# Performance work log

Hardware: AMD Instinct MI355X
Metric: run time of the kernel (lower is better)

## Reference

```python
import jax, jax.numpy as jnp
import numpy as np

SD, MD, HM, HR, N_STEPS = 64, 64, 128, 128, 10
N_VARS, DEG = 2048, 8


def _build_graph():
    rng = np.random.default_rng(0)
    n = N_VARS
    us = np.repeat(np.arange(n), 4)
    ks = np.tile(np.arange(1, 5), n)
    vs = (us + ks) % n
    factors = np.stack([np.minimum(us, vs), np.maximum(us, vs)], 1)  # [F,2], u<v
    F = factors.shape[0]
    J = np.zeros((n, n), np.float32)
    vals = rng.normal(size=F).astype(np.float32)
    J[factors[:, 0], factors[:, 1]] = vals
    J[factors[:, 1], factors[:, 0]] = vals
    b = rng.normal(size=n).astype(np.float32)
    var_node = factors.reshape(-1)          # variable of each message node
    fac_node = np.repeat(np.arange(F), 2)   # factor of each message node
    M = var_node.shape[0]
    order = np.argsort(var_node, kind='stable').reshape(n, DEG)
    jj = np.broadcast_to(order[:, :, None], (n, DEG, DEG))
    ii = np.broadcast_to(order[:, None, :], (n, DEG, DEG))
    mask = fac_node[jj] != fac_node[ii]     # same variable, different factor
    f2v_row = jj[mask].astype(np.int64)
    f2v_col = ii[mask].astype(np.int64)
    fu = fac_node[f2v_row]; fv = fac_node[f2v_col]
    feat5 = np.stack([b[var_node[f2v_col]],
                      J[factors[fu, 0], factors[fu, 1]], J[factors[fu, 1], factors[fu, 0]],
                      J[factors[fv, 0], factors[fv, 1]], J[factors[fv, 1], factors[fv, 0]]], 1).astype(np.float32)
    v2f_row = np.arange(M, dtype=np.int64)
    v2f_col = v2f_row ^ 1                   # same factor, other variable
    f = fac_node[v2f_row]
    feat4 = np.stack([b[var_node[v2f_row]], b[var_node[v2f_col]],
                      J[factors[f, 0], factors[f, 1]], J[factors[f, 1], factors[f, 0]]], 1).astype(np.float32)
    return f2v_row, f2v_col, feat5, v2f_row, v2f_col, feat4, var_node.astype(np.int64), M


def setup_inputs():
    f2v_row, f2v_col, feat5, v2f_row, v2f_col, feat4, readout_col, M = _build_graph()
    rng = np.random.default_rng(1)
    def lin(o, i):
        return rng.normal(0, 0.1, size=(o, i)).astype(np.float32), np.zeros(o, np.float32)
    def gru_p():
        s = 1.0 / np.sqrt(SD)
        return tuple(rng.uniform(-s, s, sh).astype(np.float32)
                     for sh in ((3 * SD, MD), (3 * SD, SD), (3 * SD,), (3 * SD,)))
    d = {}
    d['attn_W'], d['attn_b'] = lin(1, 2 * SD)
    d['v2f_W1'], d['v2f_b1'] = lin(HM, 2 * SD + 5)
    d['v2f_W2'], d['v2f_b2'] = lin(HM, HM)
    d['v2f_W3'], d['v2f_b3'] = lin(MD, HM)
    d['f2v_W1'], d['f2v_b1'] = lin(HM, 2 * SD + 4)
    d['f2v_W2'], d['f2v_b2'] = lin(HM, HM)
    d['f2v_W3'], d['f2v_b3'] = lin(MD, HM)
    d['ro_W1'], d['ro_b1'] = lin(HR, SD)
    d['ro_W2'], d['ro_b2'] = lin(HR, HR)
    d['ro_W3'], d['ro_b3'] = lin(2, HR)
    d['gv_Wi'], d['gv_Wh'], d['gv_bi'], d['gv_bh'] = gru_p()
    d['gf_Wi'], d['gf_Wh'], d['gf_bi'], d['gf_bh'] = gru_p()
    d = {k: jnp.asarray(v) for k, v in d.items()}
    d.update(feat5=jnp.asarray(feat5), feat4=jnp.asarray(feat4),
             f2v_row=jnp.asarray(f2v_row), f2v_col=jnp.asarray(f2v_col),
             v2f_row=jnp.asarray(v2f_row), v2f_col=jnp.asarray(v2f_col),
             readout_col=jnp.asarray(readout_col), n_vars=N_VARS, n_msg=int(M))
    return d


def _mlp3(x, W1, b1, W2, b2, W3, b3):
    h = jax.nn.relu(x @ W1.T + b1)
    h = jax.nn.relu(h @ W2.T + b2)
    return h @ W3.T + b3


def _gru(x, h, Wi, Wh, bi, bh):
    gi = x @ Wi.T + bi
    gh = h @ Wh.T + bh
    ir, iz, in_ = jnp.split(gi, 3, -1)
    hr, hz, hn = jnp.split(gh, 3, -1)
    r = jax.nn.sigmoid(ir + hr)
    z = jax.nn.sigmoid(iz + hz)
    n = jnp.tanh(in_ + r * hn)
    return (1.0 - z) * n + z * h


def reference(attn_W, attn_b, v2f_W1, v2f_b1, v2f_W2, v2f_b2, v2f_W3, v2f_b3,
              f2v_W1, f2v_b1, f2v_W2, f2v_b2, f2v_W3, f2v_b3,
              ro_W1, ro_b1, ro_W2, ro_b2, ro_W3, ro_b3,
              gv_Wi, gv_Wh, gv_bi, gv_bh, gf_Wi, gf_Wh, gf_bi, gf_bh,
              feat5, feat4, f2v_row, f2v_col, v2f_row, v2f_col, readout_col, n_vars, n_msg):
    v2f_h = jnp.zeros((n_msg, SD), feat5.dtype)
    f2v_h = jnp.zeros((n_msg, SD), feat5.dtype)

    def attn(hi, hj):
        e = jax.nn.leaky_relu(jnp.concatenate([hi, hj], -1) @ attn_W.T + attn_b)
        return jax.nn.softmax(e, axis=0)  # global softmax over all edges, shape [E,1]

    for _ in range(N_STEPS):
        hi = f2v_h[f2v_row]; hj = v2f_h[f2v_col]
        msg = _mlp3(jnp.concatenate([hi, hj, feat5], -1),
                    v2f_W1, v2f_b1, v2f_W2, v2f_b2, v2f_W3, v2f_b3) * attn(hi, hj)
        v2f_h = _gru(jax.ops.segment_sum(msg, f2v_col, num_segments=n_msg),
                     v2f_h, gv_Wi, gv_Wh, gv_bi, gv_bh)
        hi = v2f_h[v2f_row]; hj = f2v_h[v2f_col]
        msg = _mlp3(jnp.concatenate([hi, hj, feat4], -1),
                    f2v_W1, f2v_b1, f2v_W2, f2v_b2, f2v_W3, f2v_b3) * attn(hi, hj)
        f2v_h = _gru(jax.ops.segment_sum(msg, v2f_col, num_segments=n_msg),
                     f2v_h, gf_Wi, gf_Wh, gf_bi, gf_bh)

    node = jax.ops.segment_sum(f2v_h, readout_col, num_segments=n_vars)
    return jax.nn.softmax(_mlp3(node, ro_W1, ro_b1, ro_W2, ro_b2, ro_W3, ro_b3), axis=1)
```

## Files before the change

kernel.cpp:

```cpp
#include <hip/hip_runtime.h>
#include <cstdint>
#include <cstddef>

#define E1C 114688
#define MMC 16384
#define NVC 2048
#define NSTEPS 10

typedef __bf16 bf16x8 __attribute__((ext_vector_type(8)));
typedef float  f32x4  __attribute__((ext_vector_type(4)));

__device__ __forceinline__ float sigm(float x) { return 1.0f / (1.0f + expf(-x)); }
__device__ __forceinline__ bf16x8 ld8(const __bf16* p) {
  return *reinterpret_cast<const bf16x8*>(p);
}

#define NJOBS 13
struct PrepJobs {
  const float* src[NJOBS];
  __bf16* dst0;
  int kin[NJOBS];
  int nin[NJOBS];
  int ntile[NJOBS];
  int base[NJOBS];
  int total;
};

__global__ __launch_bounds__(256) void k_prep_all(PrepJobs J) {
  int gid = blockIdx.x * 256 + threadIdx.x;
  if (gid >= J.total) return;
  int jb = 0;
  #pragma unroll
  for (int x = 1; x < NJOBS; ++x) if (gid >= J.base[x]) jb = x;
  int d = gid - J.base[jb];
  int group = d >> 9, rr = d & 511, ln = rr >> 3, j = rr & 7;
  int q = ln >> 4, m16 = ln & 15;
  int NT = J.ntile[jb];
  int kc = group / NT, nt = group - kc * NT;
  int n = nt * 16 + m16, k = kc * 32 + q * 8 + j;
  int kin = J.kin[jb];
  float v = (k < kin && n < J.nin[jb]) ? J.src[jb][(size_t)n * kin + k] : 0.f;
  J.dst0[gid] = (__bf16)v;
}

template<int FDIM, int EPB, int MODE>
__global__ __launch_bounds__(256, 3) void k_mlp(
    const float* __restrict__ hA, const float* __restrict__ hB,
    const int* __restrict__ rowIdx, const int* __restrict__ colIdx,
    const float* __restrict__ feat,
    const __bf16* __restrict__ W1f, const float* __restrict__ b1,
    const __bf16* __restrict__ W2f, const float* __restrict__ b2,
    const __bf16* __restrict__ W3f, const float* __restrict__ b3,
    const float* __restrict__ attnW, const float* __restrict__ attnB,
    float* __restrict__ xout, float* __restrict__ Zpart)
{
  constexpr int RPW = EPB / 4;
  constexpr int MTILES = EPB / 16;
  constexpr int LPE = (EPB == 112) ? 2 : 4;
  constexpr int ACT = RPW * LPE;
  constexpr int ND = 128 / LPE;
  __shared__ __align__(16) __bf16 Xs[EPB][168];
  __shared__ float wexp[EPB];
  __shared__ float zp[4];
  __shared__ int mloc[16];
  const int t = threadIdx.x, lane = t & 63, w = t >> 6;
  const int r0 = w * RPW;
  const int e0 = blockIdx.x * EPB;

  {
    const int half = lane >> 5, l2 = lane & 31;
    const float* hbase = half ? hB : hA;
    const int* ibase = half ? colIdx : rowIdx;
    #pragma unroll
    for (int i = 0; i < RPW; ++i) {
      int e = r0 + i;
      int idx = ibase[e0 + e];
      float2 v = *reinterpret_cast<const float2*>(hbase + (size_t)idx * 64 + l2 * 2);
      union { __bf16 b[2]; unsigned u; } cv;
      cv.b[0] = (__bf16)v.x; cv.b[1] = (__bf16)v.y;
      *reinterpret_cast<unsigned*>(&Xs[e][half * 64 + l2 * 2]) = cv.u;
    }
    #pragma unroll
    for (int it = 0; it < RPW / 2; ++it) {
      int e = r0 + it * 2 + (lane >> 5);
      int f = lane & 31;
      float fv = (f < FDIM) ? feat[(size_t)(e0 + e) * FDIM + f] : 0.f;
      Xs[e][128 + f] = (__bf16)fv;
    }
  }

  if (MODE == 0 && t < 16) {
    int v = blockIdx.x * 2 + (t >> 3), b = t & 7;
    mloc[t] = colIdx[v * 56 + (b == 0 ? 7 : b - 1)];
  }

  {
    int eL = r0 + lane / LPE, part = lane % LPE;
    bool act = (lane < ACT);
    float s = 0.f;
    if (act) {
      #pragma unroll
      for (int jj = 0; jj < ND / 8; ++jj) {
        bf16x8 xv = ld8(&Xs[eL][part * ND + jj * 8]);
        #pragma unroll
        for (int j = 0; j < 8; ++j) s += attnW[part * ND + jj * 8 + j] * (float)xv[j];
      }
    }
    s += __shfl_xor(s, 1);
    if (LPE == 4) s += __shfl_xor(s, 2);
    float ex = 0.f;
    if (act && part == 0) {
      float le = s + attnB[0];
      le = le > 0.f ? le : 0.01f * le;
      ex = expf(le);
      wexp[eL] = ex;
    }
    #pragma unroll
    for (int off = 1; off < 64; off <<= 1) ex += __shfl_xor(ex, off);
    if (lane == 0) zp[w] = ex;
  }
  __syncthreads();
  if (t == 0) Zpart[blockIdx.x] = zp[0] + zp[1] + zp[2] + zp[3];

  const int m16 = lane & 15, q = lane >> 4;

  {
    bf16x8 B0[5], B1[5];
    #pragma unroll
    for (int kc = 0; kc < 5; ++kc) {
      B0[kc] = ld8(W1f + (size_t)(kc * 8 + w * 2 + 0) * 512 + lane * 8);
      B1[kc] = ld8(W1f + (size_t)(kc * 8 + w * 2 + 1) * 512 + lane * 8);
    }
    f32x4 a0[MTILES], a1[MTILES];
    float bv0 = b1[(w * 2) * 16 + m16], bv1 = b1[(w * 2 + 1) * 16 + m16];
    #pragma unroll
    for (int mt = 0; mt < MTILES; ++mt) {
      a0[mt] = (f32x4){bv0, bv0, bv0, bv0};
      a1[mt] = (f32x4){bv1, bv1, bv1, bv1};
      #pragma unroll
      for (int kc = 0; kc < 5; ++kc) {
        bf16x8 av = ld8(&Xs[mt * 16 + m16][kc * 32 + q * 8]);
        a0[mt] = __builtin_amdgcn_mfma_f32_16x16x32_bf16(av, B0[kc], a0[mt], 0, 0, 0);
        a1[mt] = __builtin_amdgcn_mfma_f32_16x16x32_bf16(av, B1[kc], a1[mt], 0, 0, 0);
      }
    }
    __syncthreads();
    #pragma unroll
    for (int mt = 0; mt < MTILES; ++mt)
      #pragma unroll
      for (int r2 = 0; r2 < 4; ++r2) {
        float v0 = a0[mt][r2]; v0 = v0 > 0.f ? v0 : 0.f;
        float v1 = a1[mt][r2]; v1 = v1 > 0.f ? v1 : 0.f;
        Xs[mt * 16 + q * 4 + r2][(w * 2) * 16 + m16]     = (__bf16)v0;
        Xs[mt * 16 + q * 4 + r2][(w * 2 + 1) * 16 + m16] = (__bf16)v1;
      }
    __syncthreads();
  }

  {
    bf16x8 B0[4], B1[4];
    #pragma unroll
    for (int kc = 0; kc < 4; ++kc) {
      B0[kc] = ld8(W2f + (size_t)(kc * 8 + w * 2 + 0) * 512 + lane * 8);
      B1[kc] = ld8(W2f + (size_t)(kc * 8 + w * 2 + 1) * 512 + lane * 8);
    }
    f32x4 a0[MTILES], a1[MTILES];
    float bv0 = b2[(w * 2) * 16 + m16], bv1 = b2[(w * 2 + 1) * 16 + m16];
    #pragma unroll
    for (int mt = 0; mt < MTILES; ++mt) {
      a0[mt] = (f32x4){bv0, bv0, bv0, bv0};
      a1[mt] = (f32x4){bv1, bv1, bv1, bv1};
      #pragma unroll
      for (int kc = 0; kc < 4; ++kc) {
        bf16x8 av = ld8(&Xs[mt * 16 + m16][kc * 32 + q * 8]);
        a0[mt] = __builtin_amdgcn_mfma_f32_16x16x32_bf16(av, B0[kc], a0[mt], 0, 0, 0);
        a1[mt] = __builtin_amdgcn_mfma_f32_16x16x32_bf16(av, B1[kc], a1[mt], 0, 0, 0);
      }
    }
    __syncthreads();
    #pragma unroll
    for (int mt = 0; mt < MTILES; ++mt)
      #pragma unroll
      for (int r2 = 0; r2 < 4; ++r2) {
        float v0 = a0[mt][r2]; v0 = v0 > 0.f ? v0 : 0.f;
        float v1 = a1[mt][r2]; v1 = v1 > 0.f ? v1 : 0.f;
        Xs[mt * 16 + q * 4 + r2][(w * 2) * 16 + m16]     = (__bf16)v0;
        Xs[mt * 16 + q * 4 + r2][(w * 2 + 1) * 16 + m16] = (__bf16)v1;
      }
    __syncthreads();
  }

  f32x4 a3[MTILES];
  {
    bf16x8 B3[4];
    #pragma unroll
    for (int kc = 0; kc < 4; ++kc)
      B3[kc] = ld8(W3f + (size_t)(kc * 4 + w) * 512 + lane * 8);
    float bv = b3[w * 16 + m16];
    #pragma unroll
    for (int mt = 0; mt < MTILES; ++mt) {
      a3[mt] = (f32x4){bv, bv, bv, bv};
      #pragma unroll
      for (int kc = 0; kc < 4; ++kc) {
        bf16x8 av = ld8(&Xs[mt * 16 + m16][kc * 32 + q * 8]);
        a3[mt] = __builtin_amdgcn_mfma_f32_16x16x32_bf16(av, B3[kc], a3[mt], 0, 0, 0);
      }
    }
  }
  __syncthreads();

  float* Ms = reinterpret_cast<float*>(&Xs[0][0]);
  #pragma unroll
  for (int mt = 0; mt < MTILES; ++mt)
    #pragma unroll
    for (int r2 = 0; r2 < 4; ++r2) {
      int e = mt * 16 + q * 4 + r2;
      Ms[e * 68 + w * 16 + m16] = wexp[e] * a3[mt][r2];
    }
  __syncthreads();

  if (MODE == 0) {
    int node = t >> 4, cg = t & 15;
    int vloc = node >> 3, b = node & 7;
    float4 s4 = make_float4(0.f, 0.f, 0.f, 0.f);
    #pragma unroll
    for (int a1 = 0; a1 < 7; ++a1) {
      int a = a1 + (a1 >= b ? 1 : 0);
      int e = vloc * 56 + a * 7 + b - (b > a ? 1 : 0);
      float4 mv = *reinterpret_cast<const float4*>(Ms + e * 68 + cg * 4);
      s4.x += mv.x; s4.y += mv.y; s4.z += mv.z; s4.w += mv.w;
    }
    *reinterpret_cast<float4*>(xout + (size_t)mloc[node] * 64 + cg * 4) = s4;
  } else {
    #pragma unroll
    for (int it = 0; it < 4; ++it) {
      int idx = t + it * 256;
      int ml = idx >> 4, cg = idx & 15;
      float4 v = *reinterpret_cast<const float4*>(Ms + (ml ^ 1) * 68 + cg * 4);
      *reinterpret_cast<float4*>(xout + (size_t)(e0 + ml) * 64 + cg * 4) = v;
    }
  }
}

__global__ __launch_bounds__(256, 3) void k_fuse2(
    const float* __restrict__ xt, const float* __restrict__ Zp, int zn,
    float* __restrict__ hbuf,
    const float* __restrict__ hOther,
    const float* __restrict__ feat,
    const __bf16* __restrict__ WiF, const __bf16* __restrict__ WhF,
    const float* __restrict__ bi, const float* __restrict__ bh,
    const __bf16* __restrict__ W1f, const float* __restrict__ b1,
    const __bf16* __restrict__ W2f, const float* __restrict__ b2,
    const __bf16* __restrict__ W3f, const float* __restrict__ b3,
    const float* __restrict__ attnW, const float* __restrict__ attnB,
    float* __restrict__ xout, float* __restrict__ Zpart2)
{
  __shared__ __align__(16) char smem[34880];
  __bf16* xsf = (__bf16*)smem;
  __bf16* hsf = (__bf16*)(smem + 8192);
  float (*hs32)[68] = (float (*)[68])(smem + 16384);
  __bf16 (*Xs)[168] = (__bf16 (*)[168])smem;
  float* wexp = (float*)(smem + 33792);
  float* zred = (float*)(smem + 34048);
  float* zp   = (float*)(smem + 34064);
  const int t = threadIdx.x, lane = t & 63, w = t >> 6;
  const int n0 = blockIdx.x * 64;
  const int m16 = lane & 15, q = lane >> 4;

  {
    float zs = 0.f;
    for (int i = t; i < zn; i += 256) zs += Zp[i];
    #pragma unroll
    for (int off = 32; off; off >>= 1) zs += __shfl_down(zs, off);
    if (lane == 0) zred[w] = zs;
  }
  __syncthreads();
  const float invZ = 1.0f / (zred[0] + zred[1] + zred[2] + zred[3]);

  {
    const int i = t >> 2, cb = t & 3;
    const float4* xp = (const float4*)(xt + (size_t)(n0 + i) * 64 + cb * 16);
    float4 x4[4] = {xp[0], xp[1], xp[2], xp[3]};
    #pragma unroll
    for (int k = 0; k < 4; ++k) {
      x4[k].x *= invZ; x4[k].y *= invZ; x4[k].z *= invZ; x4[k].w *= invZ;
    }
    const float* xf = (const float*)x4;
    #pragma unroll
    for (int half = 0; half < 2; ++half) {
      __bf16 v8[8];
      #pragma unroll
      for (int j = 0; j < 8; ++j) v8[j] = (__bf16)xf[half * 8 + j];
      int addr = (i >> 4) * 1024 + (cb >> 1) * 512 + ((cb & 1) * 2 + half) * 128 + (i & 15) * 8;
      *(uint4*)(xsf + addr) = *(const uint4*)v8;
    }
    const float4* hp = (const float4*)(hbuf + (size_t)(n0 + i) * 64 + cb * 16);
    float4 h4[4] = {hp[0], hp[1], hp[2], hp[3]};
    *(float4*)(&hs32[i][cb * 16 + 0])  = h4[0];
    *(float4*)(&hs32[i][cb * 16 + 4])  = h4[1];
    *(float4*)(&hs32[i][cb * 16 + 8])  = h4[2];
    *(float4*)(&hs32[i][cb * 16 + 12]) = h4[3];
    const float* hf = (const float*)h4;
    #pragma unroll
    for (int half = 0; half < 2; ++half) {
      __bf16 v8[8];
      #pragma unroll
      for (int j = 0; j < 8; ++j) v8[j] = (__bf16)hf[half * 8 + j];
      int addr = (i >> 4) * 1024 + (cb >> 1) * 512 + ((cb & 1) * 2 + half) * 128 + (i & 15) * 8;
      *(uint4*)(hsf + addr) = *(const uint4*)v8;
    }
  }
  __syncthreads();

  f32x4 gi[12], gh[12];
  #pragma unroll
  for (int nt = 0; nt < 12; ++nt) { gi[nt] = (f32x4){0,0,0,0}; gh[nt] = (f32x4){0,0,0,0}; }
  #pragma unroll
  for (int kc = 0; kc < 2; ++kc) {
    bf16x8 ax = ld8(xsf + w * 1024 + kc * 512 + lane * 8);
    bf16x8 ah = ld8(hsf + w * 1024 + kc * 512 + lane * 8);
    #pragma unroll
    for (int nt = 0; nt < 12; ++nt) {
      bf16x8 bx = ld8(WiF + (size_t)(kc * 12 + nt) * 512 + lane * 8);
      gi[nt] = __builtin_amdgcn_mfma_f32_16x16x32_bf16(ax, bx, gi[nt], 0, 0, 0);
      bf16x8 bh8 = ld8(WhF + (size_t)(kc * 12 + nt) * 512 + lane * 8);
      gh[nt] = __builtin_amdgcn_mfma_f32_16x16x32_bf16(ah, bh8, gh[nt], 0, 0, 0);
    }
  }

  float resv[4][4];
  #pragma unroll
  for (int nt = 0; nt < 4; ++nt) {
    int o = nt * 16 + m16;
    float bir = bi[o]       + bh[o];
    float biz = bi[64 + o]  + bh[64 + o];
    float bin = bi[128 + o], bhn = bh[128 + o];
    #pragma unroll
    for (int r = 0; r < 4; ++r) {
      int nl = w * 16 + q * 4 + r;
      float rg = sigm(gi[nt][r]     + gh[nt][r]     + bir);
      float zg = sigm(gi[nt + 4][r] + gh[nt + 4][r] + biz);
      float ng = tanhf(gi[nt + 8][r] + bin + rg * (gh[nt + 8][r] + bhn));
      float ho = hs32[nl][o];
      float res = (1.f - zg) * ng + zg * ho;
      resv[nt][r] = res;
      hbuf[(size_t)(n0 + nl) * 64 + o] = res;
    }
  }
  __syncthreads();

  #pragma unroll
  for (int nt = 0; nt < 4; ++nt)
    #pragma unroll
    for (int r = 0; r < 4; ++r)
      Xs[w * 16 + q * 4 + r][nt * 16 + m16] = (__bf16)resv[nt][r];
  {
    const int half = lane >> 5, l2 = lane & 31;
    #pragma unroll
    for (int i = 0; i < 16; ++i) {
      int e = w * 16 + i;
      if (half == 0) {
        float2 v = *reinterpret_cast<const float2*>(hOther + (size_t)((n0 + e) ^ 1) * 64 + l2 * 2);
        union { __bf16 b[2]; unsigned u; } cv;
        cv.b[0] = (__bf16)v.x; cv.b[1] = (__bf16)v.y;
        *reinterpret_cast<unsigned*>(&Xs[e][64 + l2 * 2]) = cv.u;
      } else {
        float fv = (l2 < 4) ? feat[(size_t)(n0 + e) * 4 + l2] : 0.f;
        Xs[e][128 + l2] = (__bf16)fv;
      }
    }
  }

  {
    int eL = w * 16 + (lane >> 2), part = lane & 3;
    float s = 0.f;
    #pragma unroll
    for (int jj = 0; jj < 4; ++jj) {
      bf16x8 xv = ld8(&Xs[eL][part * 32 + jj * 8]);
      #pragma unroll
      for (int j = 0; j < 8; ++j) s += attnW[part * 32 + jj * 8 + j] * (float)xv[j];
    }
    s += __shfl_xor(s, 1); s += __shfl_xor(s, 2);
    float ex = 0.f;
    if (part == 0) {
      float le = s + attnB[0];
      le = le > 0.f ? le : 0.01f * le;
      ex = expf(le);
      wexp[eL] = ex;
    }
    #pragma unroll
    for (int off = 1; off < 64; off <<= 1) ex += __shfl_xor(ex, off);
    if (lane == 0) zp[w] = ex;
  }
  __syncthreads();
  if (t == 0) Zpart2[blockIdx.x] = zp[0] + zp[1] + zp[2] + zp[3];

  {
    bf16x8 B0[5], B1[5];
    #pragma unroll
    for (int kc = 0; kc < 5; ++kc) {
      B0[kc] = ld8(W1f + (size_t)(kc * 8 + w * 2 + 0) * 512 + lane * 8);
      B1[kc] = ld8(W1f + (size_t)(kc * 8 + w * 2 + 1) * 512 + lane * 8);
    }
    f32x4 a0[4], a1[4];
    float bv0 = b1[(w * 2) * 16 + m16], bv1 = b1[(w * 2 + 1) * 16 + m16];
    #pragma unroll
    for (int mt = 0; mt < 4; ++mt) {
      a0[mt] = (f32x4){bv0, bv0, bv0, bv0};
      a1[mt] = (f32x4){bv1, bv1, bv1, bv1};
      #pragma unroll
      for (int kc = 0; kc < 5; ++kc) {
        bf16x8 av = ld8(&Xs[mt * 16 + m16][kc * 32 + q * 8]);
        a0[mt] = __builtin_amdgcn_mfma_f32_16x16x32_bf16(av, B0[kc], a0[mt], 0, 0, 0);
        a1[mt] = __builtin_amdgcn_mfma_f32_16x16x32_bf16(av, B1[kc], a1[mt], 0, 0, 0);
      }
    }
    __syncthreads();
    #pragma unroll
    for (int mt = 0; mt < 4; ++mt)
      #pragma unroll
      for (int r2 = 0; r2 < 4; ++r2) {
        float v0 = a0[mt][r2]; v0 = v0 > 0.f ? v0 : 0.f;
        float v1 = a1[mt][r2]; v1 = v1 > 0.f ? v1 : 0.f;
        Xs[mt * 16 + q * 4 + r2][(w * 2) * 16 + m16]     = (__bf16)v0;
        Xs[mt * 16 + q * 4 + r2][(w * 2 + 1) * 16 + m16] = (__bf16)v1;
      }
    __syncthreads();
  }

  {
    bf16x8 B0[4], B1[4];
    #pragma unroll
    for (int kc = 0; kc < 4; ++kc) {
      B0[kc] = ld8(W2f + (size_t)(kc * 8 + w * 2 + 0) * 512 + lane * 8);
      B1[kc] = ld8(W2f + (size_t)(kc * 8 + w * 2 + 1) * 512 + lane * 8);
    }
    f32x4 a0[4], a1[4];
    float bv0 = b2[(w * 2) * 16 + m16], bv1 = b2[(w * 2 + 1) * 16 + m16];
    #pragma unroll
    for (int mt = 0; mt < 4; ++mt) {
      a0[mt] = (f32x4){bv0, bv0, bv0, bv0};
      a1[mt] = (f32x4){bv1, bv1, bv1, bv1};
      #pragma unroll
      for (int kc = 0; kc < 4; ++kc) {
        bf16x8 av = ld8(&Xs[mt * 16 + m16][kc * 32 + q * 8]);
        a0[mt] = __builtin_amdgcn_mfma_f32_16x16x32_bf16(av, B0[kc], a0[mt], 0, 0, 0);
        a1[mt] = __builtin_amdgcn_mfma_f32_16x16x32_bf16(av, B1[kc], a1[mt], 0, 0, 0);
      }
    }
    __syncthreads();
    #pragma unroll
    for (int mt = 0; mt < 4; ++mt)
      #pragma unroll
      for (int r2 = 0; r2 < 4; ++r2) {
        float v0 = a0[mt][r2]; v0 = v0 > 0.f ? v0 : 0.f;
        float v1 = a1[mt][r2]; v1 = v1 > 0.f ? v1 : 0.f;
        Xs[mt * 16 + q * 4 + r2][(w * 2) * 16 + m16]     = (__bf16)v0;
        Xs[mt * 16 + q * 4 + r2][(w * 2 + 1) * 16 + m16] = (__bf16)v1;
      }
    __syncthreads();
  }

  f32x4 a3[4];
  {
    bf16x8 B3[4];
    #pragma unroll
    for (int kc = 0; kc < 4; ++kc)
      B3[kc] = ld8(W3f + (size_t)(kc * 4 + w) * 512 + lane * 8);
    float bv = b3[w * 16 + m16];
    #pragma unroll
    for (int mt = 0; mt < 4; ++mt) {
      a3[mt] = (f32x4){bv, bv, bv, bv};
      #pragma unroll
      for (int kc = 0; kc < 4; ++kc) {
        bf16x8 av = ld8(&Xs[mt * 16 + m16][kc * 32 + q * 8]);
        a3[mt] = __builtin_amdgcn_mfma_f32_16x16x32_bf16(av, B3[kc], a3[mt], 0, 0, 0);
      }
    }
  }
  __syncthreads();
  float* Ms = reinterpret_cast<float*>(&Xs[0][0]);
  #pragma unroll
  for (int mt = 0; mt < 4; ++mt)
    #pragma unroll
    for (int r2 = 0; r2 < 4; ++r2) {
      int e = mt * 16 + q * 4 + r2;
      Ms[e * 68 + w * 16 + m16] = wexp[e] * a3[mt][r2];
    }
  __syncthreads();
  #pragma unroll
  for (int it = 0; it < 4; ++it) {
    int idx = t + it * 256;
    int ml = idx >> 4, cg = idx & 15;
    float4 v = *reinterpret_cast<const float4*>(Ms + (ml ^ 1) * 68 + cg * 4);
    *reinterpret_cast<float4*>(xout + (size_t)(n0 + ml) * 64 + cg * 4) = v;
  }
}

__global__ __launch_bounds__(256) void k_gru(
    const float* __restrict__ xt, const float* __restrict__ Zp, int zn,
    float* __restrict__ hbuf,
    const __bf16* __restrict__ WiF, const __bf16* __restrict__ WhF,
    const float* __restrict__ bi, const float* __restrict__ bh)
{
  __shared__ __align__(16) __bf16 xsf[4096];
  __shared__ __align__(16) __bf16 hsf[4096];
  __shared__ float hs32[64][68];
  __shared__ float zred[4];
  const int t = threadIdx.x, lane = t & 63, w = t >> 6;
  const int n0 = blockIdx.x * 64;

  {
    float zs = 0.f;
    for (int i = t; i < zn; i += 256) zs += Zp[i];
    #pragma unroll
    for (int off = 32; off; off >>= 1) zs += __shfl_down(zs, off);
    if (lane == 0) zred[w] = zs;
  }
  __syncthreads();
  const float invZ = 1.0f / (zred[0] + zred[1] + zred[2] + zred[3]);

  {
    const int i = t >> 2, cb = t & 3;
    const float4* xp = (const float4*)(xt + (size_t)(n0 + i) * 64 + cb * 16);
    float4 x4[4] = {xp[0], xp[1], xp[2], xp[3]};
    #pragma unroll
    for (int k = 0; k < 4; ++k) {
      x4[k].x *= invZ; x4[k].y *= invZ; x4[k].z *= invZ; x4[k].w *= invZ;
    }
    const float* xf = (const float*)x4;
    #pragma unroll
    for (int half = 0; half < 2; ++half) {
      __bf16 v8[8];
      #pragma unroll
      for (int j = 0; j < 8; ++j) v8[j] = (__bf16)xf[half * 8 + j];
      int addr = (i >> 4) * 1024 + (cb >> 1) * 512 + ((cb & 1) * 2 + half) * 128 + (i & 15) * 8;
      *(uint4*)(xsf + addr) = *(const uint4*)v8;
    }
    const float4* hp = (const float4*)(hbuf + (size_t)(n0 + i) * 64 + cb * 16);
    float4 h4[4] = {hp[0], hp[1], hp[2], hp[3]};
    *(float4*)(&hs32[i][cb * 16 + 0])  = h4[0];
    *(float4*)(&hs32[i][cb * 16 + 4])  = h4[1];
    *(float4*)(&hs32[i][cb * 16 + 8])  = h4[2];
    *(float4*)(&hs32[i][cb * 16 + 12]) = h4[3];
    const float* hf = (const float*)h4;
    #pragma unroll
    for (int half = 0; half < 2; ++half) {
      __bf16 v8[8];
      #pragma unroll
      for (int j = 0; j < 8; ++j) v8[j] = (__bf16)hf[half * 8 + j];
      int addr = (i >> 4) * 1024 + (cb >> 1) * 512 + ((cb & 1) * 2 + half) * 128 + (i & 15) * 8;
      *(uint4*)(hsf + addr) = *(const uint4*)v8;
    }
  }
  __syncthreads();

  const int m16 = lane & 15, q = lane >> 4;
  f32x4 gi[12], gh[12];
  #pragma unroll
  for (int nt = 0; nt < 12; ++nt) { gi[nt] = (f32x4){0,0,0,0}; gh[nt] = (f32x4){0,0,0,0}; }
  #pragma unroll
  for (int kc = 0; kc < 2; ++kc) {
    bf16x8 ax = ld8(xsf + w * 1024 + kc * 512 + lane * 8);
    bf16x8 ah = ld8(hsf + w * 1024 + kc * 512 + lane * 8);
    #pragma unroll
    for (int nt = 0; nt < 12; ++nt) {
      bf16x8 bx = ld8(WiF + (size_t)(kc * 12 + nt) * 512 + lane * 8);
      gi[nt] = __builtin_amdgcn_mfma_f32_16x16x32_bf16(ax, bx, gi[nt], 0, 0, 0);
      bf16x8 bh8 = ld8(WhF + (size_t)(kc * 12 + nt) * 512 + lane * 8);
      gh[nt] = __builtin_amdgcn_mfma_f32_16x16x32_bf16(ah, bh8, gh[nt], 0, 0, 0);
    }
  }

  #pragma unroll
  for (int nt = 0; nt < 4; ++nt) {
    int o = nt * 16 + m16;
    float bir = bi[o]       + bh[o];
    float biz = bi[64 + o]  + bh[64 + o];
    float bin = bi[128 + o], bhn = bh[128 + o];
    #pragma unroll
    for (int r = 0; r < 4; ++r) {
      int nl = w * 16 + q * 4 + r;
      float rg = sigm(gi[nt][r]     + gh[nt][r]     + bir);
      float zg = sigm(gi[nt + 4][r] + gh[nt + 4][r] + biz);
      float ng = tanhf(gi[nt + 8][r] + bin + rg * (gh[nt + 8][r] + bhn));
      float ho = hs32[nl][o];
      hbuf[(size_t)(n0 + nl) * 64 + o] = (1.f - zg) * ng + zg * ho;
    }
  }
}

__global__ __launch_bounds__(256) void k_readout(
    const float* __restrict__ f2v_h, const int* __restrict__ f2v_col,
    const __bf16* __restrict__ W1f, const float* __restrict__ b1,
    const __bf16* __restrict__ W2f, const float* __restrict__ b2,
    const __bf16* __restrict__ W3f, const float* __restrict__ b3,
    float* __restrict__ out)
{
  __shared__ __align__(16) __bf16 Xs[64][136];
  const int t = threadIdx.x, lane = t & 63, w = t >> 6;
  const int r0 = w * 16;
  const int v0 = blockIdx.x * 64;

  #pragma unroll
  for (int i = 0; i < 16; ++i) {
    int v = v0 + r0 + i;
    float s = 0.f;
    #pragma unroll
    for (int b = 0; b < 8; ++b) {
      int m = f2v_col[v * 56 + (b == 0 ? 7 : (b - 1))];
      s += f2v_h[(size_t)m * 64 + lane];
    }
    Xs[r0 + i][lane] = (__bf16)s;
  }

  const int m16 = lane & 15, q = lane >> 4;

  {
    f32x4 acc[8];
    #pragma unroll
    for (int nt = 0; nt < 8; ++nt) {
      float bv = b1[nt * 16 + m16];
      acc[nt] = (f32x4){bv, bv, bv, bv};
    }
    #pragma unroll
    for (int kc = 0; kc < 2; ++kc) {
      bf16x8 av = ld8(&Xs[r0 + m16][kc * 32 + q * 8]);
      #pragma unroll
      for (int nt = 0; nt < 8; ++nt) {
        bf16x8 bv = ld8(W1f + (size_t)(kc * 8 + nt) * 512 + lane * 8);
        acc[nt] = __builtin_amdgcn_mfma_f32_16x16x32_bf16(av, bv, acc[nt], 0, 0, 0);
      }
    }
    #pragma unroll
    for (int nt = 0; nt < 8; ++nt)
      #pragma unroll
      for (int r2 = 0; r2 < 4; ++r2) {
        float v = acc[nt][r2]; v = v > 0.f ? v : 0.f;
        Xs[r0 + q * 4 + r2][nt * 16 + m16] = (__bf16)v;
      }
  }

  {
    f32x4 acc[8];
    #pragma unroll
    for (int nt = 0; nt < 8; ++nt) {
      float bv = b2[nt * 16 + m16];
      acc[nt] = (f32x4){bv, bv, bv, bv};
    }
    #pragma unroll
    for (int kc = 0; kc < 4; ++kc) {
      bf16x8 av = ld8(&Xs[r0 + m16][kc * 32 + q * 8]);
      #pragma unroll
      for (int nt = 0; nt < 8; ++nt) {
        bf16x8 bv = ld8(W2f + (size_t)(kc * 8 + nt) * 512 + lane * 8);
        acc[nt] = __builtin_amdgcn_mfma_f32_16x16x32_bf16(av, bv, acc[nt], 0, 0, 0);
      }
    }
    #pragma unroll
    for (int nt = 0; nt < 8; ++nt)
      #pragma unroll
      for (int r2 = 0; r2 < 4; ++r2) {
        float v = acc[nt][r2]; v = v > 0.f ? v : 0.f;
        Xs[r0 + q * 4 + r2][nt * 16 + m16] = (__bf16)v;
      }
  }

  {
    f32x4 acc = (f32x4){0, 0, 0, 0};
    if (m16 < 2) { float bv = b3[m16]; acc = (f32x4){bv, bv, bv, bv}; }
    #pragma unroll
    for (int kc = 0; kc < 4; ++kc) {
      bf16x8 av = ld8(&Xs[r0 + m16][kc * 32 + q * 8]);
      bf16x8 bv = ld8(W3f + (size_t)kc * 512 + lane * 8);
      acc = __builtin_amdgcn_mfma_f32_16x16x32_bf16(av, bv, acc, 0, 0, 0);
    }
    #pragma unroll
    for (int r = 0; r < 4; ++r) {
      float other = __shfl_xor(acc[r], 1);
      if (m16 == 0) {
        float l0 = acc[r], l1 = other;
        float mx = fmaxf(l0, l1);
        float p0 = expf(l0 - mx), p1 = expf(l1 - mx);
        float inv = 1.0f / (p0 + p1);
        int v = v0 + r0 + q * 4 + r;
        *reinterpret_cast<float2*>(out + (size_t)v * 2) = make_float2(p0 * inv, p1 * inv);
      }
    }
  }
}

extern "C" void kernel_launch(void* const* d_in, const int* in_sizes, int n_in,
                              void* d_out, int out_size, void* d_ws, size_t ws_size,
                              hipStream_t stream) {
  const float* attn_W = (const float*)d_in[0];
  const float* attn_b = (const float*)d_in[1];
  const float* v2f_W1 = (const float*)d_in[2];
  const float* v2f_b1 = (const float*)d_in[3];
  const float* v2f_W2 = (const float*)d_in[4];
  const float* v2f_b2 = (const float*)d_in[5];
  const float* v2f_W3 = (const float*)d_in[6];
  const float* v2f_b3 = (const float*)d_in[7];
  const float* f2v_W1 = (const float*)d_in[8];
  const float* f2v_b1 = (const float*)d_in[9];
  const float* f2v_W2 = (const float*)d_in[10];
  const float* f2v_b2 = (const float*)d_in[11];
  const float* f2v_W3 = (const float*)d_in[12];
  const float* f2v_b3 = (const float*)d_in[13];
  const float* ro_W1  = (const float*)d_in[14];
  const float* ro_b1  = (const float*)d_in[15];
  const float* ro_W2  = (const float*)d_in[16];
  const float* ro_b2  = (const float*)d_in[17];
  const float* ro_W3  = (const float*)d_in[18];
  const float* ro_b3  = (const float*)d_in[19];
  const float* gv_Wi  = (const float*)d_in[20];
  const float* gv_Wh  = (const float*)d_in[21];
  const float* gv_bi  = (const float*)d_in[22];
  const float* gv_bh  = (const float*)d_in[23];
  const float* gf_Wi  = (const float*)d_in[24];
  const float* gf_Wh  = (const float*)d_in[25];
  const float* gf_bi  = (const float*)d_in[26];
  const float* gf_bh  = (const float*)d_in[27];
  const float* feat5  = (const float*)d_in[28];
  const float* feat4  = (const float*)d_in[29];
  const int* f2v_row  = (const int*)d_in[30];
  const int* f2v_col  = (const int*)d_in[31];
  const int* v2f_row  = (const int*)d_in[32];
  const int* v2f_col  = (const int*)d_in[33];

  float* ws = (float*)d_ws;
  float* xt1    = ws;
  float* xt2    = xt1 + (size_t)MMC * 64;
  float* h_v2f  = xt2 + (size_t)MMC * 64;
  float* h_f2v  = h_v2f + (size_t)MMC * 64;
  float* Zp     = h_f2v + (size_t)MMC * 64;
  __bf16* wbuf  = (__bf16*)(((uintptr_t)(Zp + 20 * 1024) + 15) & ~(uintptr_t)15);
  __bf16* w1v = wbuf;
  __bf16* w2v = w1v + 20480;
  __bf16* w3v = w2v + 16384;
  __bf16* w1f = w3v + 8192;
  __bf16* w2f = w1f + 20480;
  __bf16* w3f = w2f + 16384;
  __bf16* wiv = w3f + 8192;
  __bf16* whv = wiv + 12288;
  __bf16* wif = whv + 12288;
  __bf16* whf = wif + 12288;
  __bf16* wr1 = whf + 12288;
  __bf16* wr2 = wr1 + 8192;
  __bf16* wr3 = wr2 + 16384;

  hipMemsetAsync(h_v2f, 0, (size_t)2 * MMC * 64 * sizeof(float), stream);

  {
    PrepJobs J;
    const float* srcs[NJOBS] = {v2f_W1, v2f_W2, v2f_W3, f2v_W1, f2v_W2, f2v_W3,
                                gv_Wi, gv_Wh, gf_Wi, gf_Wh, ro_W1, ro_W2, ro_W3};
    int kin[NJOBS]  = {133, 128, 128, 132, 128, 128, 64, 64, 64, 64, 64, 128, 128};
    int nin[NJOBS]  = {128, 128, 64, 128, 128, 64, 192, 192, 192, 192, 128, 128, 2};
    int nt[NJOBS]   = {8, 8, 4, 8, 8, 4, 12, 12, 12, 12, 8, 8, 1};
    int size[NJOBS] = {20480, 16384, 8192, 20480, 16384, 8192,
                       12288, 12288, 12288, 12288, 8192, 16384, 2048};
    int cum = 0;
    for (int i = 0; i < NJOBS; ++i) {
      J.src[i] = srcs[i]; J.kin[i] = kin[i]; J.nin[i] = nin[i]; J.ntile[i] = nt[i];
      J.base[i] = cum; cum += size[i];
    }
    J.dst0 = wbuf; J.total = cum;
    k_prep_all<<<(cum + 255) / 256, 256, 0, stream>>>(J);
  }

  const int ZN1 = E1C / 112;
  const int ZN2 = MMC / 64;

  for (int s = 0; s < NSTEPS; ++s) {
    float* z1 = Zp + (size_t)(s * 2) * 1024;
    float* z2 = Zp + (size_t)(s * 2 + 1) * 1024;
    k_mlp<5, 112, 0><<<E1C / 112, 256, 0, stream>>>(
        h_f2v, h_v2f, f2v_row, f2v_col, feat5,
        w1v, v2f_b1, w2v, v2f_b2, w3v, v2f_b3,
        attn_W, attn_b, xt1, z1);
    k_fuse2<<<MMC / 64, 256, 0, stream>>>(
        xt1, z1, ZN1, h_v2f, h_f2v, feat4,
        wiv, whv, gv_bi, gv_bh,
        w1f, f2v_b1, w2f, f2v_b2, w3f, f2v_b3,
        attn_W, attn_b, xt2, z2);
    k_gru<<<MMC / 64, 256, 0, stream>>>(xt2, z2, ZN2, h_f2v,
                                        wif, whf, gf_bi, gf_bh);
  }
  k_readout<<<NVC / 64, 256, 0, stream>>>(h_f2v, f2v_col,
                                          wr1, ro_b1, wr2, ro_b2, wr3, ro_b3,
                                          (float*)d_out);
}
```

Measured before the change: 701.3 us.

## Split attention out of GRU kernel and fuse f2v MLP with second GRU

Restructures the per-step kernel boundaries. The first GRU kernel now also computes the f2v attention logits and partial sums and writes them to a small buffer. A new kernel then runs the f2v MLP and feeds its messages directly into the second GRU through shared memory, so the xt2 intermediate no longer makes a global round trip. The attention dot product now runs in fp32 from shared memory and global reads, and the second GRU reduces a fixed 256-entry partial array. In exchange the fused kernel uses more shared memory and registers, which may lower occupancy.

```diff
diff --git a/kernel.cpp b/kernel.cpp
--- a/kernel.cpp
+++ b/kernel.cpp
@@ -232,8 +232,9 @@
     }
     *reinterpret_cast<float4*>(xout + (size_t)mloc[node] * 64 + cg * 4) = s4;
   } else {
-    #pragma unroll
-    for (int it = 0; it < 4; ++it) {
+    constexpr int WIT = (EPB * 16) / 256;
+    #pragma unroll
+    for (int it = 0; it < WIT; ++it) {
       int idx = t + it * 256;
       int ml = idx >> 4, cg = idx & 15;
       float4 v = *reinterpret_cast<const float4*>(Ms + (ml ^ 1) * 68 + cg * 4);
@@ -242,30 +243,21 @@
   }
 }
 
-__global__ __launch_bounds__(256, 3) void k_fuse2(
+__global__ __launch_bounds__(256) void k_gru_att(
     const float* __restrict__ xt, const float* __restrict__ Zp, int zn,
-    float* __restrict__ hbuf,
-    const float* __restrict__ hOther,
-    const float* __restrict__ feat,
+    float* __restrict__ hbuf, const float* __restrict__ hOther,
+    const float* __restrict__ attnW, const float* __restrict__ attnB,
     const __bf16* __restrict__ WiF, const __bf16* __restrict__ WhF,
     const float* __restrict__ bi, const float* __restrict__ bh,
-    const __bf16* __restrict__ W1f, const float* __restrict__ b1,
-    const __bf16* __restrict__ W2f, const float* __restrict__ b2,
-    const __bf16* __restrict__ W3f, const float* __restrict__ b3,
-    const float* __restrict__ attnW, const float* __restrict__ attnB,
-    float* __restrict__ xout, float* __restrict__ Zpart2)
+    float* __restrict__ eatt2, float* __restrict__ Zp2)
 {
-  __shared__ __align__(16) char smem[34880];
-  __bf16* xsf = (__bf16*)smem;
-  __bf16* hsf = (__bf16*)(smem + 8192);
-  float (*hs32)[68] = (float (*)[68])(smem + 16384);
-  __bf16 (*Xs)[168] = (__bf16 (*)[168])smem;
-  float* wexp = (float*)(smem + 33792);
-  float* zred = (float*)(smem + 34048);
-  float* zp   = (float*)(smem + 34064);
+  __shared__ __align__(16) __bf16 xsf[4096];
+  __shared__ __align__(16) __bf16 hsf[4096];
+  __shared__ float hs32[64][68];
+  __shared__ float zred[4];
+  __shared__ float zp2s[4];
   const int t = threadIdx.x, lane = t & 63, w = t >> 6;
   const int n0 = blockIdx.x * 64;
-  const int m16 = lane & 15, q = lane >> 4;
 
   {
     float zs = 0.f;
@@ -312,6 +304,7 @@
   }
   __syncthreads();
 
+  const int m16 = lane & 15, q = lane >> 4;
   f32x4 gi[12], gh[12];
   #pragma unroll
   for (int nt = 0; nt < 12; ++nt) { gi[nt] = (f32x4){0,0,0,0}; gh[nt] = (f32x4){0,0,0,0}; }
@@ -328,7 +321,6 @@
     }
   }
 
-  float resv[4][4];
   #pragma unroll
   for (int nt = 0; nt < 4; ++nt) {
     int o = nt * 16 + m16;
@@ -343,42 +335,22 @@
       float ng = tanhf(gi[nt + 8][r] + bin + rg * (gh[nt + 8][r] + bhn));
       float ho = hs32[nl][o];
       float res = (1.f - zg) * ng + zg * ho;
-      resv[nt][r] = res;
       hbuf[(size_t)(n0 + nl) * 64 + o] = res;
-    }
-  }
-  __syncthreads();
-
-  #pragma unroll
-  for (int nt = 0; nt < 4; ++nt)
-    #pragma unroll
-    for (int r = 0; r < 4; ++r)
-      Xs[w * 16 + q * 4 + r][nt * 16 + m16] = (__bf16)resv[nt][r];
-  {
-    const int half = lane >> 5, l2 = lane & 31;
-    #pragma unroll
-    for (int i = 0; i < 16; ++i) {
-      int e = w * 16 + i;
-      if (half == 0) {
-        float2 v = *reinterpret_cast<const float2*>(hOther + (size_t)((n0 + e) ^ 1) * 64 + l2 * 2);
-        union { __bf16 b[2]; unsigned u; } cv;
-        cv.b[0] = (__bf16)v.x; cv.b[1] = (__bf16)v.y;
-        *reinterpret_cast<unsigned*>(&Xs[e][64 + l2 * 2]) = cv.u;
-      } else {
-        float fv = (l2 < 4) ? feat[(size_t)(n0 + e) * 4 + l2] : 0.f;
-        Xs[e][128 + l2] = (__bf16)fv;
-      }
-    }
-  }
-
-  {
-    int eL = w * 16 + (lane >> 2), part = lane & 3;
+      hs32[nl][o] = res;
+    }
+  }
+  __syncthreads();
+
+  {
+    int e = w * 16 + (lane >> 2), part = lane & 3;
     float s = 0.f;
-    #pragma unroll
-    for (int jj = 0; jj < 4; ++jj) {
-      bf16x8 xv = ld8(&Xs[eL][part * 32 + jj * 8]);
-      #pragma unroll
-      for (int j = 0; j < 8; ++j) s += attnW[part * 32 + jj * 8 + j] * (float)xv[j];
+    if (part < 2) {
+      #pragma unroll
+      for (int j = 0; j < 32; ++j) s += attnW[part * 32 + j] * hs32[e][part * 32 + j];
+    } else {
+      const float* hj = hOther + (size_t)((n0 + e) ^ 1) * 64 + (part - 2) * 32;
+      #pragma unroll
+      for (int j = 0; j < 32; ++j) s += attnW[64 + (part - 2) * 32 + j] * hj[j];
     }
     s += __shfl_xor(s, 1); s += __shfl_xor(s, 2);
     float ex = 0.f;
@@ -386,14 +358,75 @@
       float le = s + attnB[0];
       le = le > 0.f ? le : 0.01f * le;
       ex = expf(le);
-      wexp[eL] = ex;
-    }
-    #pragma unroll
-    for (int off = 1; off < 64; off <<= 1) ex += __shfl_xor(ex, off);
-    if (lane == 0) zp[w] = ex;
-  }
-  __syncthreads();
-  if (t == 0) Zpart2[blockIdx.x] = zp[0] + zp[1] + zp[2] + zp[3];
+      eatt2[n0 + e] = ex;
+    }
+    #pragma unroll
+    for (int off = 4; off < 64; off <<= 1) ex += __shfl_xor(ex, off);
+    if (lane == 0) zp2s[w] = ex;
+  }
+  __syncthreads();
+  if (t == 0) Zp2[blockIdx.x] = zp2s[0] + zp2s[1] + zp2s[2] + zp2s[3];
+}
+
+__global__ __launch_bounds__(256) void k_fuse(
+    const float* __restrict__ hV, float* __restrict__ hF,
+    const float* __restrict__ feat,
+    const float* __restrict__ eatt2, const float* __restrict__ Zp2,
+    const __bf16* __restrict__ W1f, const float* __restrict__ b1,
+    const __bf16* __restrict__ W2f, const float* __restrict__ b2,
+    const __bf16* __restrict__ W3f, const float* __restrict__ b3,
+    const __bf16* __restrict__ WiF, const __bf16* __restrict__ WhF,
+    const float* __restrict__ bi, const float* __restrict__ bh)
+{
+  __shared__ __align__(16) __bf16 Xs[64][168];
+  __shared__ __align__(16) float hs32[64][68];
+  __shared__ __align__(16) __bf16 xsf[4096];
+  __shared__ __align__(16) __bf16 hsf[4096];
+  __shared__ float wexp[64];
+  __shared__ float zred[4];
+  const int t = threadIdx.x, lane = t & 63, w = t >> 6;
+  const int n0 = blockIdx.x * 64;
+  const int m16 = lane & 15, q = lane >> 4;
+
+  {
+    float zs = Zp2[t];
+    #pragma unroll
+    for (int off = 32; off; off >>= 1) zs += __shfl_down(zs, off);
+    if (lane == 0) zred[w] = zs;
+  }
+  if (t < 64) wexp[t] = eatt2[n0 + t];
+
+  {
+    const int half = lane >> 5, l2 = lane & 31;
+    const int r0 = w * 16;
+    #pragma unroll
+    for (int i = 0; i < 16; ++i) {
+      int e = r0 + i;
+      const float* src = half ? (hF + (size_t)((n0 + e) ^ 1) * 64)
+                              : (hV + (size_t)(n0 + e) * 64);
+      float2 v = *reinterpret_cast<const float2*>(src + l2 * 2);
+      union { __bf16 b[2]; unsigned u; } cv;
+      cv.b[0] = (__bf16)v.x; cv.b[1] = (__bf16)v.y;
+      *reinterpret_cast<unsigned*>(&Xs[e][half * 64 + l2 * 2]) = cv.u;
+    }
+    #pragma unroll
+    for (int it = 0; it < 8; ++it) {
+      int e = r0 + it * 2 + (lane >> 5);
+      int f = lane & 31;
+      float fv = (f < 4) ? feat[(size_t)(n0 + e) * 4 + f] : 0.f;
+      Xs[e][128 + f] = (__bf16)fv;
+    }
+  }
+  {
+    const int i = t >> 2, cb = t & 3;
+    const float4* hp = (const float4*)(hF + (size_t)(n0 + i) * 64 + cb * 16);
+    *(float4*)(&hs32[i][cb * 16 + 0])  = hp[0];
+    *(float4*)(&hs32[i][cb * 16 + 4])  = hp[1];
+    *(float4*)(&hs32[i][cb * 16 + 8])  = hp[2];
+    *(float4*)(&hs32[i][cb * 16 + 12]) = hp[3];
+  }
+  __syncthreads();
+  const float invZ = 1.0f / (zred[0] + zred[1] + zred[2] + zred[3]);
 
   {
     bf16x8 B0[5], B1[5];
@@ -488,74 +521,35 @@
       Ms[e * 68 + w * 16 + m16] = wexp[e] * a3[mt][r2];
     }
   __syncthreads();
-  #pragma unroll
-  for (int it = 0; it < 4; ++it) {
-    int idx = t + it * 256;
-    int ml = idx >> 4, cg = idx & 15;
-    float4 v = *reinterpret_cast<const float4*>(Ms + (ml ^ 1) * 68 + cg * 4);
-    *reinterpret_cast<float4*>(xout + (size_t)(n0 + ml) * 64 + cg * 4) = v;
-  }
-}
-
-__global__ __launch_bounds__(256) void k_gru(
-    const float* __restrict__ xt, const float* __restrict__ Zp, int zn,
-    float* __restrict__ hbuf,
-    const __bf16* __restrict__ WiF, const __bf16* __restrict__ WhF,
-    const float* __restrict__ bi, const float* __restrict__ bh)
-{
-  __shared__ __align__(16) __bf16 xsf[4096];
-  __shared__ __align__(16) __bf16 hsf[4096];
-  __shared__ float hs32[64][68];
-  __shared__ float zred[4];
-  const int t = threadIdx.x, lane = t & 63, w = t >> 6;
-  const int n0 = blockIdx.x * 64;
-
-  {
-    float zs = 0.f;
-    for (int i = t; i < zn; i += 256) zs += Zp[i];
-    #pragma unroll
-    for (int off = 32; off; off >>= 1) zs += __shfl_down(zs, off);
-    if (lane == 0) zred[w] = zs;
-  }
-  __syncthreads();
-  const float invZ = 1.0f / (zred[0] + zred[1] + zred[2] + zred[3]);
 
   {
     const int i = t >> 2, cb = t & 3;
-    const float4* xp = (const float4*)(xt + (size_t)(n0 + i) * 64 + cb * 16);
-    float4 x4[4] = {xp[0], xp[1], xp[2], xp[3]};
-    #pragma unroll
-    for (int k = 0; k < 4; ++k) {
-      x4[k].x *= invZ; x4[k].y *= invZ; x4[k].z *= invZ; x4[k].w *= invZ;
-    }
-    const float* xf = (const float*)x4;
+    float x16[16];
+    #pragma unroll
+    for (int k4 = 0; k4 < 4; ++k4) {
+      float4 v = *reinterpret_cast<const float4*>(Ms + (i ^ 1) * 68 + cb * 16 + k4 * 4);
+      x16[k4 * 4 + 0] = v.x * invZ; x16[k4 * 4 + 1] = v.y * invZ;
+      x16[k4 * 4 + 2] = v.z * invZ; x16[k4 * 4 + 3] = v.w * invZ;
+    }
     #pragma unroll
     for (int half = 0; half < 2; ++half) {
       __bf16 v8[8];
       #pragma unroll
-      for (int j = 0; j < 8; ++j) v8[j] = (__bf16)xf[half * 8 + j];
+      for (int j = 0; j < 8; ++j) v8[j] = (__bf16)x16[half * 8 + j];
       int addr = (i >> 4) * 1024 + (cb >> 1) * 512 + ((cb & 1) * 2 + half) * 128 + (i & 15) * 8;
       *(uint4*)(xsf + addr) = *(const uint4*)v8;
     }
-    const float4* hp = (const float4*)(hbuf + (size_t)(n0 + i) * 64 + cb * 16);
-    float4 h4[4] = {hp[0], hp[1], hp[2], hp[3]};
-    *(float4*)(&hs32[i][cb * 16 + 0])  = h4[0];
-    *(float4*)(&hs32[i][cb * 16 + 4])  = h4[1];
-    *(float4*)(&hs32[i][cb * 16 + 8])  = h4[2];
-    *(float4*)(&hs32[i][cb * 16 + 12]) = h4[3];
-    const float* hf = (const float*)h4;
     #pragma unroll
     for (int half = 0; half < 2; ++half) {
       __bf16 v8[8];
       #pragma unroll
-      for (int j = 0; j < 8; ++j) v8[j] = (__bf16)hf[half * 8 + j];
+      for (int j = 0; j < 8; ++j) v8[j] = (__bf16)hs32[i][cb * 16 + half * 8 + j];
       int addr = (i >> 4) * 1024 + (cb >> 1) * 512 + ((cb & 1) * 2 + half) * 128 + (i & 15) * 8;
       *(uint4*)(hsf + addr) = *(const uint4*)v8;
     }
   }
   __syncthreads();
 
-  const int m16 = lane & 15, q = lane >> 4;
   f32x4 gi[12], gh[12];
   #pragma unroll
   for (int nt = 0; nt < 12; ++nt) { gi[nt] = (f32x4){0,0,0,0}; gh[nt] = (f32x4){0,0,0,0}; }
@@ -585,7 +579,7 @@
       float zg = sigm(gi[nt + 4][r] + gh[nt + 4][r] + biz);
       float ng = tanhf(gi[nt + 8][r] + bin + rg * (gh[nt + 8][r] + bhn));
       float ho = hs32[nl][o];
-      hbuf[(size_t)(n0 + nl) * 64 + o] = (1.f - zg) * ng + zg * ho;
+      hF[(size_t)(n0 + nl) * 64 + o] = (1.f - zg) * ng + zg * ho;
     }
   }
 }
@@ -725,16 +719,15 @@
   const float* feat4  = (const float*)d_in[29];
   const int* f2v_row  = (const int*)d_in[30];
   const int* f2v_col  = (const int*)d_in[31];
-  const int* v2f_row  = (const int*)d_in[32];
-  const int* v2f_col  = (const int*)d_in[33];
 
   float* ws = (float*)d_ws;
   float* xt1    = ws;
-  float* xt2    = xt1 + (size_t)MMC * 64;
-  float* h_v2f  = xt2 + (size_t)MMC * 64;
+  float* h_v2f  = xt1 + (size_t)MMC * 64;
   float* h_f2v  = h_v2f + (size_t)MMC * 64;
-  float* Zp     = h_f2v + (size_t)MMC * 64;
-  __bf16* wbuf  = (__bf16*)(((uintptr_t)(Zp + 20 * 1024) + 15) & ~(uintptr_t)15);
+  float* Zp1    = h_f2v + (size_t)MMC * 64;
+  float* Zp2    = Zp1 + 1024;
+  float* eatt2  = Zp2 + 256;
+  __bf16* wbuf  = (__bf16*)(((uintptr_t)(eatt2 + MMC) + 15) & ~(uintptr_t)15);
   __bf16* w1v = wbuf;
   __bf16* w2v = w1v + 20480;
   __bf16* w3v = w2v + 16384;
@@ -770,22 +763,19 @@
   }
 
   const int ZN1 = E1C / 112;
-  const int ZN2 = MMC / 64;
 
   for (int s = 0; s < NSTEPS; ++s) {
-    float* z1 = Zp + (size_t)(s * 2) * 1024;
-    float* z2 = Zp + (size_t)(s * 2 + 1) * 1024;
     k_mlp<5, 112, 0><<<E1C / 112, 256, 0, stream>>>(
         h_f2v, h_v2f, f2v_row, f2v_col, feat5,
         w1v, v2f_b1, w2v, v2f_b2, w3v, v2f_b3,
-        attn_W, attn_b, xt1, z1);
-    k_fuse2<<<MMC / 64, 256, 0, stream>>>(
-        xt1, z1, ZN1, h_v2f, h_f2v, feat4,
-        wiv, whv, gv_bi, gv_bh,
+        attn_W, attn_b, xt1, Zp1);
+    k_gru_att<<<MMC / 64, 256, 0, stream>>>(
+        xt1, Zp1, ZN1, h_v2f, h_f2v, attn_W, attn_b,
+        wiv, whv, gv_bi, gv_bh, eatt2, Zp2);
+    k_fuse<<<MMC / 64, 256, 0, stream>>>(
+        h_v2f, h_f2v, feat4, eatt2, Zp2,
         w1f, f2v_b1, w2f, f2v_b2, w3f, f2v_b3,
-        attn_W, attn_b, xt2, z2);
-    k_gru<<<MMC / 64, 256, 0, stream>>>(xt2, z2, ZN2, h_f2v,
-                                        wif, whf, gf_bi, gf_bh);
+        wif, whf, gf_bi, gf_bh);
   }
   k_readout<<<NVC / 64, 256, 0, stream>>>(h_f2v, f2v_col,
                                           wr1, ro_b1, wr2, ro_b2, wr3, ro_b3,
```

Measured after the change: 659.2 us, median of 2. 6.0% less time.
